# Kernel optimization log

Hardware: AMD Instinct MI355X
Metric: run time of the kernel (lower is better)

The kernel has to match this reference:

```python
import jax, jax.numpy as jnp
import numpy as np

DIM = 1024
HEADS = 16
HEAD_DIM = DIM // HEADS
DFF = 4 * DIM  # SwiGLU expansion=4.0
EPS = 1e-5
NEG = -1e4  # original uses -1e4 causal mask, not -inf


def rms_norm(x, w):
    v = jnp.mean(x * x, axis=-1, keepdims=True)
    return w * (x * jax.lax.rsqrt(v + EPS))


def rotate_half(x):
    x1, x2 = jnp.split(x, 2, axis=-1)
    return jnp.concatenate((-x2, x1), axis=-1)


def setup_inputs() -> dict:
    key = jax.random.key(0)
    ks = jax.random.split(key, 12)
    B, S = 2, 2048
    s = 0.02
    h = jax.random.normal(ks[0], (B, S, DIM), jnp.float32)
    # RoPE tables, half-split convention: emb = concat(freqs, freqs)
    inv_freq = 1.0 / (10000.0 ** (np.arange(0, HEAD_DIM, 2, dtype=np.float32) / HEAD_DIM))
    freqs = np.arange(S, dtype=np.float32)[:, None] * inv_freq[None, :]
    emb = np.concatenate([freqs, freqs], axis=-1)
    cos = jnp.asarray(np.cos(emb))  # [S, HEAD_DIM]
    sin = jnp.asarray(np.sin(emb))
    return {
        "h": h, "cos": cos, "sin": sin,
        "norm1_w": jnp.ones((DIM,), jnp.float32),
        "wq": jax.random.normal(ks[1], (DIM, DIM), jnp.float32) * s,
        "wk": jax.random.normal(ks[2], (DIM, DIM), jnp.float32) * s,
        "wv": jax.random.normal(ks[3], (DIM, DIM), jnp.float32) * s,
        "wo": jax.random.normal(ks[4], (DIM, DIM), jnp.float32) * s,
        "norm2_w": jnp.ones((DIM,), jnp.float32),
        "gate_w": jax.random.normal(ks[5], (DFF, DIM), jnp.float32) * s,
        "gate_b": jnp.zeros((DFF,), jnp.float32),
        "up_w": jax.random.normal(ks[6], (DFF, DIM), jnp.float32) * s,
        "up_b": jnp.zeros((DFF,), jnp.float32),
        "down_w": jax.random.normal(ks[7], (DIM, DFF), jnp.float32) * s,
        "down_b": jnp.zeros((DIM,), jnp.float32),
        "gate": jnp.full((DIM,), 0.5, jnp.float32),
    }


def reference(h, cos, sin, norm1_w, wq, wk, wv, wo, norm2_w,
              gate_w, gate_b, up_w, up_b, down_w, down_b, gate):
    B, S, _ = h.shape
    scale = HEAD_DIM ** -0.5

    x = rms_norm(h, norm1_w)

    def heads(t):  # [B,S,DIM] -> [B,H,S,D]
        return t.reshape(B, S, HEADS, HEAD_DIM).transpose(0, 2, 1, 3)

    q = heads(x @ wq.T)
    k = heads(x @ wk.T)
    v = heads(x @ wv.T)

    # inline RoPE (cos/sin broadcast [S,D] over [B,H,S,D])
    q = q * cos + rotate_half(q) * sin
    k = k * cos + rotate_half(k) * sin

    scores = jnp.einsum('bhsd,bhtd->bhst', q, k) * scale
    causal = jnp.triu(jnp.full((S, S), NEG, jnp.float32), k=1)
    scores = scores + causal
    attn = jax.nn.softmax(scores, axis=-1)
    out = jnp.einsum('bhst,bhtd->bhsd', attn, v)
    out = out.transpose(0, 2, 1, 3).reshape(B, S, DIM)
    attn_out = out @ wo.T

    h = h + attn_out

    x2 = rms_norm(h, norm2_w)
    g = jax.nn.silu(x2 @ gate_w.T + gate_b)
    u = x2 @ up_w.T + up_b
    mlp = (g * u) @ down_w.T + down_b

    h = h + jax.nn.sigmoid(gate) * mlp
    return h
```

## Files before the change

### kernel.cpp

```cpp
#include <hip/hip_runtime.h>
#include <math.h>

#define DIM    1024
#define HEADS  16
#define HD     64
#define SEQ    2048
#define BATCH  2
#define TTOK   4096
#define DFF    4096
#define S3     3072

typedef __attribute__((ext_vector_type(8))) short short8;
typedef __attribute__((ext_vector_type(4))) float f32x4;

__device__ __forceinline__ float bf2f(unsigned short u) {
  union { unsigned int u; float f; } v; v.u = ((unsigned int)u) << 16; return v.f;
}
__device__ __forceinline__ unsigned short f2bf(float f) {
  union { float f; unsigned int u; } v; v.f = f;
  return (unsigned short)((v.u + 0x7FFFu + ((v.u >> 16) & 1u)) >> 16);
}
__device__ __forceinline__ unsigned short f2bf_trunc(float f) {
  union { float f; unsigned int u; } v; v.f = f;
  return (unsigned short)(v.u >> 16);
}

#define AS1(p) ((const __attribute__((address_space(1))) void*)(p))
#define AS3(p) ((__attribute__((address_space(3))) void*)(p))

__global__ __launch_bounds__(256) void wconv_k(
    const float* __restrict__ s0, const float* __restrict__ s1,
    const float* __restrict__ s2, const float* __restrict__ s3,
    const float* __restrict__ s4, const float* __restrict__ s5,
    const float* __restrict__ s6, unsigned short* __restrict__ dst)
{
  const int i = blockIdx.x * 256 + threadIdx.x;
  const float* s; int base;
  if (i < 1048576) {
    if (i < 524288) { if (i < 262144) { s = s0; base = 0; } else { s = s1; base = 262144; } }
    else            { if (i < 786432) { s = s2; base = 524288; } else { s = s3; base = 786432; } }
  } else if (i < 2097152) { s = s4; base = 1048576; }
  else if (i < 3145728)   { s = s5; base = 2097152; }
  else                    { s = s6; base = 3145728; }
  const float4 f = ((const float4*)s)[i - base];
  unsigned long long o = (unsigned long long)f2bf(f.x)
                       | ((unsigned long long)f2bf(f.y) << 16)
                       | ((unsigned long long)f2bf(f.z) << 32)
                       | ((unsigned long long)f2bf(f.w) << 48);
  ((unsigned long long*)dst)[i] = o;
}

template<int MODE>
__global__ __launch_bounds__(256) void gemm_bt(
    const unsigned short* __restrict__ A,
    const unsigned short* __restrict__ W,
    unsigned short* __restrict__ C,
    float* __restrict__ Cf,
    const float* __restrict__ resf,
    const float* __restrict__ cosp,
    const float* __restrict__ sinp,
    int M, int N, int K)
{
  __shared__ __align__(16) unsigned short As[128 * 64];
  __shared__ __align__(16) unsigned short Bs[128 * 64];

  const int tid  = threadIdx.x;
  const int lane = tid & 63;
  const int wv   = tid >> 6;
  const int row0 = blockIdx.x * 128;
  const int col0 = blockIdx.y * 128;
  const int wm   = (wv >> 1) * 64;
  const int wn   = (wv & 1) * 64;
  const int lr   = lane & 15;
  const int lg   = lane >> 4;

  const int srow = lane >> 3;
  const int skg  = (lane & 7) ^ srow;

  int kb = 0, ke = K;
  if (MODE == 6) { kb = blockIdx.z * 1024; ke = kb + 1024; }

  f32x4 acc[4][4];
#pragma unroll
  for (int i = 0; i < 4; i++)
#pragma unroll
    for (int j = 0; j < 4; j++) acc[i][j] = (f32x4){0.f, 0.f, 0.f, 0.f};

  for (int k0 = kb; k0 < ke; k0 += 64) {
#pragma unroll
    for (int i = 0; i < 4; i++) {
      const int c = wv * 4 + i;
      const unsigned short* ga = A + (size_t)(row0 + c * 8 + srow) * K + k0 + skg * 8;
      __builtin_amdgcn_global_load_lds(AS1(ga), AS3(As + c * 512), 16, 0, 0);
      const unsigned short* gb = W + (size_t)(col0 + c * 8 + srow) * K + k0 + skg * 8;
      __builtin_amdgcn_global_load_lds(AS1(gb), AS3(Bs + c * 512), 16, 0, 0);
    }
    __syncthreads();

#pragma unroll
    for (int ks = 0; ks < 2; ks++) {
      short8 af[4], bf[4];
#pragma unroll
      for (int i = 0; i < 4; i++) {
        const int r = wm + i * 16 + lr;
        af[i] = *(const short8*)(As + r * 64 + (((ks * 4 + lg) ^ (lr & 7)) * 8));
      }
#pragma unroll
      for (int j = 0; j < 4; j++) {
        const int r = wn + j * 16 + lr;
        bf[j] = *(const short8*)(Bs + r * 64 + (((ks * 4 + lg) ^ (lr & 7)) * 8));
      }
#pragma unroll
      for (int i = 0; i < 4; i++)
#pragma unroll
        for (int j = 0; j < 4; j++)
          acc[i][j] = __builtin_amdgcn_mfma_f32_16x16x32_bf16(af[i], bf[j], acc[i][j], 0, 0, 0);
    }
    __syncthreads();
  }

  if (MODE == 5) {
    const bool do_rope = (col0 < 2048);
#pragma unroll
    for (int i = 0; i < 4; i++) {
#pragma unroll
      for (int r = 0; r < 4; r++) {
        const int row = row0 + wm + i * 16 + lg * 4 + r;
        const int s = row & (SEQ - 1);
        const size_t rb = (size_t)row * N + col0 + wn;
        if (do_rope) {
#pragma unroll
          for (int jp = 0; jp < 2; jp++) {
            const int d = jp * 16 + lr;
            const float c = cosp[s * HD + d];
            const float sn = sinp[s * HD + d];
            const float x1v = acc[i][jp][r];
            const float x2v = acc[i][jp + 2][r];
            C[rb + d]      = f2bf(x1v * c - x2v * sn);
            C[rb + d + 32] = f2bf(x2v * c + x1v * sn);
          }
        } else {
#pragma unroll
          for (int j = 0; j < 4; j++)
            C[rb + j * 16 + lr] = f2bf(acc[i][j][r]);
        }
      }
    }
    return;
  }

  unsigned short* Cz = C;
  if (MODE == 6) {
    const size_t pz[4] = {4u * 1048576u, 8u * 1048576u, 16u * 1048576u, 0u};
    Cz = C + pz[blockIdx.z];
  }
#pragma unroll
  for (int i = 0; i < 4; i++) {
#pragma unroll
    for (int j = 0; j < 4; j++) {
      const int col = col0 + wn + j * 16 + lr;
#pragma unroll
      for (int r = 0; r < 4; r++) {
        const int row = row0 + wm + i * 16 + lg * 4 + r;
        const float v = acc[i][j][r];
        const size_t idx = (size_t)row * N + col;
        if (MODE == 3) {
          Cf[idx] = v + resf[idx];
        } else if (MODE == 6) {
          Cz[idx] = f2bf(v);
        }
      }
    }
  }
}

__global__ __launch_bounds__(256) void dcomb_k(
    const unsigned short* __restrict__ ws, float* __restrict__ out,
    const float* __restrict__ db, const float* __restrict__ gate)
{
  const int i4 = blockIdx.x * 256 + threadIdx.x;
  const size_t idx = (size_t)i4 * 4;
  const int col = (int)(idx & 1023);
  const unsigned long long p0 = *(const unsigned long long*)(ws + 4u * 1048576u + idx);
  const unsigned long long p1 = *(const unsigned long long*)(ws + 8u * 1048576u + idx);
  const unsigned long long p2 = *(const unsigned long long*)(ws + 16u * 1048576u + idx);
  const unsigned long long p3 = *(const unsigned long long*)(ws + idx);
  float4 o = *(float4*)(out + idx);
  float* op = (float*)&o;
#pragma unroll
  for (int w = 0; w < 4; w++) {
    const float s = bf2f((unsigned short)(p0 >> (16 * w)))
                  + bf2f((unsigned short)(p1 >> (16 * w)))
                  + bf2f((unsigned short)(p2 >> (16 * w)))
                  + bf2f((unsigned short)(p3 >> (16 * w)))
                  + db[col + w];
    const float sg = 1.0f / (1.0f + __expf(-gate[col + w]));
    op[w] += sg * s;
  }
  *(float4*)(out + idx) = o;
}

__global__ __launch_bounds__(256) void gemm_swiglu(
    const unsigned short* __restrict__ A,
    const unsigned short* __restrict__ Wg,
    const unsigned short* __restrict__ Wu,
    unsigned short* __restrict__ G,
    const float* __restrict__ gb,
    const float* __restrict__ ub,
    int M, int N, int K)
{
  __shared__ __align__(16) unsigned short As[128 * 64];
  __shared__ __align__(16) unsigned short Gs[128 * 64];
  __shared__ __align__(16) unsigned short Us[128 * 64];

  const int tid  = threadIdx.x;
  const int lane = tid & 63;
  const int wv   = tid >> 6;
  const int row0 = blockIdx.x * 128;
  const int col0 = blockIdx.y * 128;
  const int wm   = (wv >> 1) * 64;
  const int wn   = (wv & 1) * 64;
  const int lr   = lane & 15;
  const int lg   = lane >> 4;

  const int srow = lane >> 3;
  const int skg  = (lane & 7) ^ srow;

  f32x4 ag[4][4], au[4][4];
#pragma unroll
  for (int i = 0; i < 4; i++)
#pragma unroll
    for (int j = 0; j < 4; j++) {
      ag[i][j] = (f32x4){0.f, 0.f, 0.f, 0.f};
      au[i][j] = (f32x4){0.f, 0.f, 0.f, 0.f};
    }

  for (int k0 = 0; k0 < K; k0 += 64) {
#pragma unroll
    for (int i = 0; i < 4; i++) {
      const int c = wv * 4 + i;
      const unsigned short* ga = A + (size_t)(row0 + c * 8 + srow) * K + k0 + skg * 8;
      __builtin_amdgcn_global_load_lds(AS1(ga), AS3(As + c * 512), 16, 0, 0);
      const unsigned short* gg = Wg + (size_t)(col0 + c * 8 + srow) * K + k0 + skg * 8;
      __builtin_amdgcn_global_load_lds(AS1(gg), AS3(Gs + c * 512), 16, 0, 0);
      const unsigned short* gu = Wu + (size_t)(col0 + c * 8 + srow) * K + k0 + skg * 8;
      __builtin_amdgcn_global_load_lds(AS1(gu), AS3(Us + c * 512), 16, 0, 0);
    }
    __syncthreads();

#pragma unroll
    for (int ks = 0; ks < 2; ks++) {
      short8 af[4], bg[4], bu[4];
#pragma unroll
      for (int i = 0; i < 4; i++) {
        const int r = wm + i * 16 + lr;
        af[i] = *(const short8*)(As + r * 64 + (((ks * 4 + lg) ^ (lr & 7)) * 8));
      }
#pragma unroll
      for (int j = 0; j < 4; j++) {
        const int r = wn + j * 16 + lr;
        const int off = (((ks * 4 + lg) ^ (lr & 7)) * 8);
        bg[j] = *(const short8*)(Gs + r * 64 + off);
        bu[j] = *(const short8*)(Us + r * 64 + off);
      }
#pragma unroll
      for (int i = 0; i < 4; i++)
#pragma unroll
        for (int j = 0; j < 4; j++) {
          ag[i][j] = __builtin_amdgcn_mfma_f32_16x16x32_bf16(af[i], bg[j], ag[i][j], 0, 0, 0);
          au[i][j] = __builtin_amdgcn_mfma_f32_16x16x32_bf16(af[i], bu[j], au[i][j], 0, 0, 0);
        }
    }
    __syncthreads();
  }

#pragma unroll
  for (int i = 0; i < 4; i++) {
#pragma unroll
    for (int j = 0; j < 4; j++) {
      const int col = col0 + wn + j * 16 + lr;
#pragma unroll
      for (int r = 0; r < 4; r++) {
        const int row = row0 + wm + i * 16 + lg * 4 + r;
        float g = ag[i][j][r] + gb[col];
        g = g / (1.0f + __expf(-g));
        const float u = au[i][j][r] + ub[col];
        G[(size_t)row * N + col] = f2bf(g * u);
      }
    }
  }
}

template<int XF32>
__global__ __launch_bounds__(256) void rmsnorm_k(
    const void* __restrict__ Xv,
    const float* __restrict__ W,
    unsigned short* __restrict__ Y)
{
  const int t  = blockIdx.x;
  const int i0 = threadIdx.x * 4;

  float v[4];
  if (XF32) {
    const float4 f = *(const float4*)((const float*)Xv + (size_t)t * DIM + i0);
    v[0] = f.x; v[1] = f.y; v[2] = f.z; v[3] = f.w;
  } else {
    unsigned long long raw = *(const unsigned long long*)((const unsigned short*)Xv + (size_t)t * DIM + i0);
#pragma unroll
    for (int k = 0; k < 4; k++) v[k] = bf2f((unsigned short)(raw >> (16 * k)));
  }

  float ss = v[0] * v[0] + v[1] * v[1] + v[2] * v[2] + v[3] * v[3];
#pragma unroll
  for (int off = 32; off > 0; off >>= 1) ss += __shfl_xor(ss, off);

  __shared__ float red[4];
  if ((threadIdx.x & 63) == 0) red[threadIdx.x >> 6] = ss;
  __syncthreads();
  const float tot = red[0] + red[1] + red[2] + red[3];
  const float r = rsqrtf(tot * (1.0f / DIM) + 1e-5f);

  const float4 wf = *(const float4*)(W + i0);
  const float wv4[4] = {wf.x, wf.y, wf.z, wf.w};
  unsigned long long o = 0;
#pragma unroll
  for (int k = 0; k < 4; k++)
    o |= ((unsigned long long)f2bf(v[k] * r * wv4[k])) << (16 * k);
  *(unsigned long long*)(Y + (size_t)t * DIM + i0) = o;
}

__device__ const unsigned char cqt[32] = {10,10,15,15,9,9,13,14,14,14,15,4,8,8,12,12,13,13,7,7,11,11,11,12,3,6,6,5,5,2,1,0};
__device__ const unsigned char ctb[32] = {0,11,0,11,0,10,0,0,10,20,22,0,0,9,0,9,10,19,0,8,0,8,16,18,0,0,7,0,6,0,0,0};
__device__ const unsigned char ccnt[32] = {11,11,11,11,10,10,10,10,10,10,10,10,9,9,9,9,9,9,8,8,8,8,8,8,8,7,7,6,6,6,4,2};
__device__ const unsigned char cchv[32] = {0,1,0,1,0,1,0,0,1,2,2,0,0,1,0,1,1,2,0,1,0,1,2,2,0,0,1,0,1,0,0,0};
__device__ const unsigned char cpsv[32] = {255,5,255,14,255,4,255,255,12,13,15,255,255,3,255,8,10,11,255,2,255,6,7,9,255,255,1,255,0,255,255,255};

__global__ __launch_bounds__(256) void fattn_k(
    const unsigned short* __restrict__ QKV,
    unsigned short* __restrict__ O,
    unsigned short* __restrict__ Pbuf,
    float* __restrict__ Lbuf)
{
  __shared__ __align__(16) unsigned short Ks[2][64 * 64];
  __shared__ __align__(16) unsigned short Vt[2][64 * 72];
  __shared__ __align__(16) unsigned short Ps[4 * 32 * 72];

  const int tid  = threadIdx.x;
  const int lane = tid & 63;
  const int wv   = tid >> 6;
  const int lr   = lane & 15;
  const int lg   = lane >> 4;

  const int j  = blockIdx.x;
  const int bh = blockIdx.y;
  const int qt = cqt[j];
  const int tb = ctb[j];
  const int nt = ccnt[j];
  const int ch = cchv[j];
  const int ps = cpsv[j];
  const int b  = bh >> 4, h = bh & 15;
  const int q0 = qt * 128;
  const size_t rowb = (size_t)b * SEQ;
  const int qoff = h * HD;
  const int koff = 1024 + qoff;
  const int voff = 2048 + qoff;

  short8 aq[2][2];
#pragma unroll
  for (int rf = 0; rf < 2; rf++) {
    const size_t tok = rowb + q0 + wv * 32 + rf * 16 + lr;
    aq[rf][0] = *(const short8*)(QKV + tok * S3 + qoff + lg * 8);
    aq[rf][1] = *(const short8*)(QKV + tok * S3 + qoff + 32 + lg * 8);
  }

  f32x4 o[2][4];
  f32x4 lacc[2];
#pragma unroll
  for (int rf = 0; rf < 2; rf++) {
    lacc[rf] = (f32x4){0.f, 0.f, 0.f, 0.f};
#pragma unroll
    for (int d = 0; d < 4; d++) o[rf][d] = (f32x4){0.f, 0.f, 0.f, 0.f};
  }
  short8 onesb;
#pragma unroll
  for (int jj = 0; jj < 8; jj++) onesb[jj] = (short)0x3F80;

  const int srow = lane >> 3;
  const int skg  = (lane & 7) ^ srow;
  const int kv   = tid >> 2;
  const int d0   = (tid & 3) * 16;

  const float C1 = 0.125f * 1.44269504f;
  const float C2 = 11.5415603f;

  auto stage = [&](int buf, int ti) {
    const int t0 = (tb + ti) * 64;
    unsigned short* ksb = &Ks[buf][0];
#pragma unroll
    for (int i = 0; i < 2; i++) {
      const int c = wv * 2 + i;
      const unsigned short* gk = QKV + (rowb + t0 + c * 8 + srow) * S3 + koff + skg * 8;
      __builtin_amdgcn_global_load_lds(AS1(gk), AS3(ksb + c * 512), 16, 0, 0);
    }
    unsigned short* vtb = &Vt[buf][0];
    const unsigned short* gv = QKV + (rowb + t0 + kv) * S3 + voff + d0;
    const short8 v0 = *(const short8*)gv;
    const short8 v1 = *(const short8*)(gv + 8);
    const int klo = kv & 7, khi = kv >> 3;
#pragma unroll
    for (int w = 0; w < 8; w++) {
      const int da = d0 + w, db2 = d0 + 8 + w;
      vtb[da  * 72 + ((khi ^ ((da  >> 3) & 7)) * 8) + klo] = (unsigned short)v0[w];
      vtb[db2 * 72 + ((khi ^ ((db2 >> 3) & 7)) * 8) + klo] = (unsigned short)v1[w];
    }
  };

  stage(0, 0);

  for (int ti = 0; ti < nt; ti++) {
    __syncthreads();
    if (ti + 1 < nt) stage((ti + 1) & 1, ti + 1);

    const int t0 = (tb + ti) * 64;
    const unsigned short* ksb = &Ks[ti & 1][0];
    const unsigned short* vtb = &Vt[ti & 1][0];

    f32x4 S[2][4];
#pragma unroll
    for (int sub = 0; sub < 4; sub++) {
      const int kr = sub * 16 + lr;
      const short8 bk0 = *(const short8*)(ksb + kr * 64 + ((lg       ^ (kr & 7)) * 8));
      const short8 bk1 = *(const short8*)(ksb + kr * 64 + (((4 + lg) ^ (kr & 7)) * 8));
#pragma unroll
      for (int rf = 0; rf < 2; rf++) {
        f32x4 s = (f32x4){0.f, 0.f, 0.f, 0.f};
        s = __builtin_amdgcn_mfma_f32_16x16x32_bf16(aq[rf][0], bk0, s, 0, 0, 0);
        s = __builtin_amdgcn_mfma_f32_16x16x32_bf16(aq[rf][1], bk1, s, 0, 0, 0);
        S[rf][sub] = s;
      }
    }

    unsigned short* pw = Ps + wv * (32 * 72);
#pragma unroll
    for (int rf = 0; rf < 2; rf++) {
      const int qmin = q0 + wv * 32 + rf * 16;
      const bool diag = (t0 + 63 > qmin);
#pragma unroll
      for (int sub = 0; sub < 4; sub++) {
#pragma unroll
        for (int r = 0; r < 4; r++) {
          float t = fmaf(S[rf][sub][r], C1, -C2);
          if (diag && (t0 + sub * 16 + lr > qmin + lg * 4 + r)) t = -INFINITY;
          const float p = exp2f(t);
          pw[(rf * 16 + lg * 4 + r) * 72 + sub * 16 + lr] = f2bf_trunc(p);
        }
      }
    }

#pragma unroll
    for (int kf = 0; kf < 2; kf++) {
      const short8 pa0 = *(const short8*)(pw + lr * 72 + kf * 32 + lg * 8);
      const short8 pa1 = *(const short8*)(pw + (16 + lr) * 72 + kf * 32 + lg * 8);
      lacc[0] = __builtin_amdgcn_mfma_f32_16x16x32_bf16(pa0, onesb, lacc[0], 0, 0, 0);
      lacc[1] = __builtin_amdgcn_mfma_f32_16x16x32_bf16(pa1, onesb, lacc[1], 0, 0, 0);
#pragma unroll
      for (int dsub = 0; dsub < 4; dsub++) {
        const int d = dsub * 16 + lr;
        const short8 bvf = *(const short8*)(vtb + d * 72 +
                             (((kf * 4 + lg) ^ ((d >> 3) & 7)) * 8));
        o[0][dsub] = __builtin_amdgcn_mfma_f32_16x16x32_bf16(pa0, bvf, o[0][dsub], 0, 0, 0);
        o[1][dsub] = __builtin_amdgcn_mfma_f32_16x16x32_bf16(pa1, bvf, o[1][dsub], 0, 0, 0);
      }
    }
  }

  if (ps == 255 && qt < 5) {
#pragma unroll
    for (int rf = 0; rf < 2; rf++) {
      float inv[4];
#pragma unroll
      for (int r = 0; r < 4; r++) inv[r] = 1.0f / lacc[rf][r];
#pragma unroll
      for (int dsub = 0; dsub < 4; dsub++)
#pragma unroll
        for (int r = 0; r < 4; r++)
          O[(rowb + q0 + wv * 32 + rf * 16 + lg * 4 + r) * DIM + h * HD + dsub * 16 + lr] =
              f2bf(o[rf][dsub][r] * inv[r]);
    }
  } else {
    const int lbase = ((bh * 11 + (qt - 5)) * 3 + ch) * 128;
#pragma unroll
    for (int rf = 0; rf < 2; rf++) {
      const int rbase = wv * 32 + rf * 16 + lg * 4;
      if (lr == 0) {
#pragma unroll
        for (int r = 0; r < 4; r++) Lbuf[lbase + rbase + r] = lacc[rf][r];
      }
    }
    if (ps == 255) {
#pragma unroll
      for (int rf = 0; rf < 2; rf++)
#pragma unroll
        for (int dsub = 0; dsub < 4; dsub++)
#pragma unroll
          for (int r = 0; r < 4; r++)
            O[(rowb + q0 + wv * 32 + rf * 16 + lg * 4 + r) * DIM + h * HD + dsub * 16 + lr] =
                f2bf(o[rf][dsub][r]);
    } else {
      unsigned short* pb = Pbuf + ((size_t)bh * 16 + ps) * 8192;
#pragma unroll
      for (int rf = 0; rf < 2; rf++) {
        const int rbase = wv * 32 + rf * 16 + lg * 4;
#pragma unroll
        for (int dsub = 0; dsub < 4; dsub++)
#pragma unroll
          for (int r = 0; r < 4; r++)
            pb[(rbase + r) * 64 + dsub * 16 + lr] = f2bf(o[rf][dsub][r]);
      }
    }
  }
}

__global__ __launch_bounds__(256) void fattn_combine_k(
    const unsigned short* __restrict__ Pbuf,
    const float* __restrict__ Lbuf,
    unsigned short* __restrict__ O)
{
  const int qt = 5 + blockIdx.x;
  const int bh = blockIdx.y;
  const int b  = bh >> 4, h = bh & 15;
  const int q0 = qt * 128;
  const size_t rowb = (size_t)b * SEQ;
  const int pbase_t[11] = {0, 1, 2, 3, 4, 5, 6, 8, 10, 12, 14};
  const int pb0 = pbase_t[qt - 5];
  const int np  = (qt < 11) ? 1 : 2;
  const int lbase = (bh * 11 + (qt - 5)) * 3 * 128;

  const unsigned short* p0 = Pbuf + ((size_t)bh * 16 + pb0) * 8192;
  const unsigned short* p1 = Pbuf + ((size_t)bh * 16 + pb0 + 1) * 8192;

#pragma unroll
  for (int it = 0; it < 4; it++) {
    const int idx = it * 2048 + threadIdx.x * 8;
    const int row = idx >> 6;
    const int col = idx & 63;
    float ls = Lbuf[lbase + row] + Lbuf[lbase + 128 + row];
    if (np == 2) ls += Lbuf[lbase + 256 + row];
    const float inv = 1.0f / ls;

    unsigned short* op = O + (rowb + q0 + row) * DIM + h * HD + col;
    const short8 vb = *(const short8*)op;
    const short8 e0 = *(const short8*)(p0 + idx);
    short8 e1;
    if (np == 2) e1 = *(const short8*)(p1 + idx);
    short8 r;
#pragma unroll
    for (int w = 0; w < 8; w++) {
      float s = bf2f((unsigned short)vb[w]) + bf2f((unsigned short)e0[w]);
      if (np == 2) s += bf2f((unsigned short)e1[w]);
      r[w] = (short)f2bf(s * inv);
    }
    *(short8*)op = r;
  }
}

extern "C" void kernel_launch(void* const* d_in, const int* in_sizes, int n_in,
                              void* d_out, int out_size, void* d_ws, size_t ws_size,
                              hipStream_t stream)
{
  const float* h    = (const float*)d_in[0];
  const float* cosb = (const float*)d_in[1];
  const float* sinb = (const float*)d_in[2];
  const float* n1w  = (const float*)d_in[3];
  const float* n2w  = (const float*)d_in[8];
  const float* gb   = (const float*)d_in[10];
  const float* ub   = (const float*)d_in[12];
  const float* db   = (const float*)d_in[14];
  const float* gatep= (const float*)d_in[15];
  float* out = (float*)d_out;

  unsigned short* ws = (unsigned short*)d_ws;
  const size_t M1 = 1u << 20;

  unsigned short* wqkv = ws;
  unsigned short* wo_c = ws + 3 * M1;
  unsigned short* gw_c = ws + 4 * M1;
  unsigned short* uw_c = ws + 8 * M1;
  unsigned short* dw_c = ws + 12 * M1;
  unsigned short* x1   = ws + 16 * M1;
  unsigned short* Pbuf = ws + 16 * M1;
  unsigned short* x2   = ws + 16 * M1;
  float*          Lbuf = (float*)ws;
  unsigned short* qkv  = ws + 20 * M1;
  unsigned short* attn = ws + 32 * M1;
  unsigned short* g    = qkv;

  const dim3 blk(256);
  const dim3 gq(TTOK / 128, S3 / 128);
  const dim3 g1(TTOK / 128, DIM / 128);
  const dim3 g2(TTOK / 128, DFF / 128);
  const dim3 gd(TTOK / 128, DIM / 128, 4);

  wconv_k<<<16384, blk, 0, stream>>>(
      (const float*)d_in[4], (const float*)d_in[5], (const float*)d_in[6],
      (const float*)d_in[7], (const float*)d_in[9], (const float*)d_in[11],
      (const float*)d_in[13], ws);

  rmsnorm_k<1><<<TTOK, blk, 0, stream>>>(h, n1w, x1);

  gemm_bt<5><<<gq, blk, 0, stream>>>(x1, wqkv, qkv, nullptr, nullptr,
                                     cosb, sinb, TTOK, S3, DIM);

  fattn_k<<<dim3(32, BATCH * HEADS), blk, 0, stream>>>(qkv, attn, Pbuf, Lbuf);
  fattn_combine_k<<<dim3(11, BATCH * HEADS), blk, 0, stream>>>(Pbuf, Lbuf, attn);

  gemm_bt<3><<<g1, blk, 0, stream>>>(attn, wo_c, nullptr, out, h,
                                     nullptr, nullptr, TTOK, DIM, DIM);

  rmsnorm_k<1><<<TTOK, blk, 0, stream>>>(out, n2w, x2);

  gemm_swiglu<<<g2, blk, 0, stream>>>(x2, gw_c, uw_c, g, gb, ub, TTOK, DFF, DIM);

  gemm_bt<6><<<gd, blk, 0, stream>>>(g, dw_c, ws, nullptr, nullptr,
                                     nullptr, nullptr, TTOK, DIM, DFF);

  dcomb_k<<<4096, blk, 0, stream>>>(ws, out, db, gatep);
}
```

Before: 473.1 us.

## Interleave gate/up weights and compute SwiGLU via generic GEMM epilogue

The weight conversion kernel now writes gate and up weights interleaved in 16-row groups into one 8192x1024 matrix. The dedicated dual-accumulator SwiGLU GEMM is removed, and the generic 128x128 GEMM gets a new epilogue mode that pairs adjacent 16-column fragments as gate/up and applies SiLU and the multiply. The old kernel held 32 accumulator tiles per thread and used three LDS buffers, so this is meant to cut register pressure and raise occupancy. The cost is twice as many blocks, each reloading the activation tile, so total A traffic doubles.

```diff
diff --git a/kernel.cpp b/kernel.cpp
--- a/kernel.cpp
+++ b/kernel.cpp
@@ -35,19 +35,27 @@
     const float* __restrict__ s6, unsigned short* __restrict__ dst)
 {
   const int i = blockIdx.x * 256 + threadIdx.x;
-  const float* s; int base;
+  const float* s; int base; int di = i;
   if (i < 1048576) {
     if (i < 524288) { if (i < 262144) { s = s0; base = 0; } else { s = s1; base = 262144; } }
     else            { if (i < 786432) { s = s2; base = 524288; } else { s = s3; base = 786432; } }
-  } else if (i < 2097152) { s = s4; base = 1048576; }
-  else if (i < 3145728)   { s = s5; base = 2097152; }
-  else                    { s = s6; base = 3145728; }
+  } else if (i < 2097152) {
+    s = s4; base = 1048576;
+    const int u = i - base; const int r = u >> 8; const int c = u & 255;
+    di = 1048576 + (((r >> 4) << 5) + (r & 15)) * 256 + c;
+  } else if (i < 3145728) {
+    s = s5; base = 2097152;
+    const int u = i - base; const int r = u >> 8; const int c = u & 255;
+    di = 1048576 + (((r >> 4) << 5) + 16 + (r & 15)) * 256 + c;
+  } else {
+    s = s6; base = 3145728;
+  }
   const float4 f = ((const float4*)s)[i - base];
   unsigned long long o = (unsigned long long)f2bf(f.x)
                        | ((unsigned long long)f2bf(f.y) << 16)
                        | ((unsigned long long)f2bf(f.z) << 32)
                        | ((unsigned long long)f2bf(f.w) << 48);
-  ((unsigned long long*)dst)[i] = o;
+  ((unsigned long long*)dst)[di] = o;
 }
 
 template<int MODE>
@@ -149,6 +157,28 @@
     return;
   }
 
+  if (MODE == 7) {
+    const int cb = (col0 + wn) >> 1;
+#pragma unroll
+    for (int i = 0; i < 4; i++) {
+#pragma unroll
+      for (int jp = 0; jp < 2; jp++) {
+        const int lcol = cb + jp * 16 + lr;
+        const float gbv = resf[lcol];
+        const float ubv = cosp[lcol];
+#pragma unroll
+        for (int r = 0; r < 4; r++) {
+          const int row = row0 + wm + i * 16 + lg * 4 + r;
+          float gv = acc[i][2 * jp][r] + gbv;
+          gv = gv / (1.0f + __expf(-gv));
+          const float uv = acc[i][2 * jp + 1][r] + ubv;
+          C[(size_t)row * DFF + lcol] = f2bf(gv * uv);
+        }
+      }
+    }
+    return;
+  }
+
   unsigned short* Cz = C;
   if (MODE == 6) {
     const size_t pz[4] = {4u * 1048576u, 8u * 1048576u, 16u * 1048576u, 0u};
@@ -198,97 +228,6 @@
     op[w] += sg * s;
   }
   *(float4*)(out + idx) = o;
-}
-
-__global__ __launch_bounds__(256) void gemm_swiglu(
-    const unsigned short* __restrict__ A,
-    const unsigned short* __restrict__ Wg,
-    const unsigned short* __restrict__ Wu,
-    unsigned short* __restrict__ G,
-    const float* __restrict__ gb,
-    const float* __restrict__ ub,
-    int M, int N, int K)
-{
-  __shared__ __align__(16) unsigned short As[128 * 64];
-  __shared__ __align__(16) unsigned short Gs[128 * 64];
-  __shared__ __align__(16) unsigned short Us[128 * 64];
-
-  const int tid  = threadIdx.x;
-  const int lane = tid & 63;
-  const int wv   = tid >> 6;
-  const int row0 = blockIdx.x * 128;
-  const int col0 = blockIdx.y * 128;
-  const int wm   = (wv >> 1) * 64;
-  const int wn   = (wv & 1) * 64;
-  const int lr   = lane & 15;
-  const int lg   = lane >> 4;
-
-  const int srow = lane >> 3;
-  const int skg  = (lane & 7) ^ srow;
-
-  f32x4 ag[4][4], au[4][4];
-#pragma unroll
-  for (int i = 0; i < 4; i++)
-#pragma unroll
-    for (int j = 0; j < 4; j++) {
-      ag[i][j] = (f32x4){0.f, 0.f, 0.f, 0.f};
-      au[i][j] = (f32x4){0.f, 0.f, 0.f, 0.f};
-    }
-
-  for (int k0 = 0; k0 < K; k0 += 64) {
-#pragma unroll
-    for (int i = 0; i < 4; i++) {
-      const int c = wv * 4 + i;
-      const unsigned short* ga = A + (size_t)(row0 + c * 8 + srow) * K + k0 + skg * 8;
-      __builtin_amdgcn_global_load_lds(AS1(ga), AS3(As + c * 512), 16, 0, 0);
-      const unsigned short* gg = Wg + (size_t)(col0 + c * 8 + srow) * K + k0 + skg * 8;
-      __builtin_amdgcn_global_load_lds(AS1(gg), AS3(Gs + c * 512), 16, 0, 0);
-      const unsigned short* gu = Wu + (size_t)(col0 + c * 8 + srow) * K + k0 + skg * 8;
-      __builtin_amdgcn_global_load_lds(AS1(gu), AS3(Us + c * 512), 16, 0, 0);
-    }
-    __syncthreads();
-
-#pragma unroll
-    for (int ks = 0; ks < 2; ks++) {
-      short8 af[4], bg[4], bu[4];
-#pragma unroll
-      for (int i = 0; i < 4; i++) {
-        const int r = wm + i * 16 + lr;
-        af[i] = *(const short8*)(As + r * 64 + (((ks * 4 + lg) ^ (lr & 7)) * 8));
-      }
-#pragma unroll
-      for (int j = 0; j < 4; j++) {
-        const int r = wn + j * 16 + lr;
-        const int off = (((ks * 4 + lg) ^ (lr & 7)) * 8);
-        bg[j] = *(const short8*)(Gs + r * 64 + off);
-        bu[j] = *(const short8*)(Us + r * 64 + off);
-      }
-#pragma unroll
-      for (int i = 0; i < 4; i++)
-#pragma unroll
-        for (int j = 0; j < 4; j++) {
-          ag[i][j] = __builtin_amdgcn_mfma_f32_16x16x32_bf16(af[i], bg[j], ag[i][j], 0, 0, 0);
-          au[i][j] = __builtin_amdgcn_mfma_f32_16x16x32_bf16(af[i], bu[j], au[i][j], 0, 0, 0);
-        }
-    }
-    __syncthreads();
-  }
-
-#pragma unroll
-  for (int i = 0; i < 4; i++) {
-#pragma unroll
-    for (int j = 0; j < 4; j++) {
-      const int col = col0 + wn + j * 16 + lr;
-#pragma unroll
-      for (int r = 0; r < 4; r++) {
-        const int row = row0 + wm + i * 16 + lg * 4 + r;
-        float g = ag[i][j][r] + gb[col];
-        g = g / (1.0f + __expf(-g));
-        const float u = au[i][j][r] + ub[col];
-        G[(size_t)row * N + col] = f2bf(g * u);
-      }
-    }
-  }
 }
 
 template<int XF32>
@@ -584,8 +523,7 @@
 
   unsigned short* wqkv = ws;
   unsigned short* wo_c = ws + 3 * M1;
-  unsigned short* gw_c = ws + 4 * M1;
-  unsigned short* uw_c = ws + 8 * M1;
+  unsigned short* gu_c = ws + 4 * M1;
   unsigned short* dw_c = ws + 12 * M1;
   unsigned short* x1   = ws + 16 * M1;
   unsigned short* Pbuf = ws + 16 * M1;
@@ -598,7 +536,7 @@
   const dim3 blk(256);
   const dim3 gq(TTOK / 128, S3 / 128);
   const dim3 g1(TTOK / 128, DIM / 128);
-  const dim3 g2(TTOK / 128, DFF / 128);
+  const dim3 g2(TTOK / 128, (2 * DFF) / 128);
   const dim3 gd(TTOK / 128, DIM / 128, 4);
 
   wconv_k<<<16384, blk, 0, stream>>>(
@@ -619,7 +557,8 @@
 
   rmsnorm_k<1><<<TTOK, blk, 0, stream>>>(out, n2w, x2);
 
-  gemm_swiglu<<<g2, blk, 0, stream>>>(x2, gw_c, uw_c, g, gb, ub, TTOK, DFF, DIM);
+  gemm_bt<7><<<g2, blk, 0, stream>>>(x2, gu_c, g, nullptr, gb,
+                                     ub, nullptr, TTOK, 2 * DFF, DIM);
 
   gemm_bt<6><<<gd, blk, 0, stream>>>(g, dw_c, ws, nullptr, nullptr,
                                      nullptr, nullptr, TTOK, DIM, DFF);
```

Result: faster. 445.8 us (-5.8%).
